# Kernel optimization log

Measured on AMD Instinct MI355X. Metric: run time of the kernel, lower is better.

## Reference

```python
import jax, jax.numpy as jnp
import numpy as np

B, S, D, H = 2, 2048, 1024, 16
DK = D // H


def setup_inputs() -> dict:
    key = jax.random.key(0)
    ks = jax.random.split(key, 12)
    sc = 1.0 / np.sqrt(D)
    return {
        "q": jax.random.normal(ks[0], (B, S, D), jnp.float32),
        "k": jax.random.normal(ks[1], (B, S, D), jnp.float32),
        "v": jax.random.normal(ks[2], (B, S, D), jnp.float32),
        "mask": jax.random.randint(ks[3], (B, S), 0, 2, jnp.int32),
        "Wq": jax.random.normal(ks[4], (D, D), jnp.float32) * sc,
        "bq": jnp.zeros((D,), jnp.float32),
        "Wk": jax.random.normal(ks[5], (D, D), jnp.float32) * sc,
        "bk": jnp.zeros((D,), jnp.float32),
        "Wv": jax.random.normal(ks[6], (D, D), jnp.float32) * sc,
        "bv": jnp.zeros((D,), jnp.float32),
        "Wo": jax.random.normal(ks[7], (D, D), jnp.float32) * sc,
        "bo": jnp.zeros((D,), jnp.float32),
    }


def reference(q, k, v, mask, Wq, bq, Wk, bk, Wv, bv, Wo, bo):
    # Projections (flax nn.Dense: x @ W + b)
    query = q @ Wq + bq          # [B,S,D]
    key_ = k @ Wk + bk
    value = v @ Wv + bv
    # split heads -> [B,H,S,DK]
    def split(x):
        return x.reshape(B, S, H, DK).transpose(0, 2, 1, 3)
    qh, kh, vh = split(query), split(key_), split(value)
    scores = jnp.einsum('bhqd,bhkd->bhqk', qh, kh) / jnp.sqrt(jnp.float32(DK))
    # Faithful to source: mask=(mask==0); where(mask==0, -1e10, scores)
    # i.e. positions where ORIGINAL mask != 0 are set to -1e10.
    m = (mask == 0)[:, None, None, :]          # [B,1,1,S] bool
    scores = jnp.where(~m, jnp.float32(-1e10), scores)
    attn = jax.nn.softmax(scores, axis=-1)     # dropout deterministic (eval)
    x = jnp.einsum('bhqk,bhkd->bhqd', attn, vh)
    x = x.transpose(0, 2, 1, 3).reshape(B, S, D)
    return x @ Wo + bo
```

## Files before the change

kernel.cpp:

```cpp
#include <hip/hip_runtime.h>
#include <hip/hip_bf16.h>

typedef unsigned short u16;
typedef unsigned int u32;
typedef __attribute__((ext_vector_type(8))) __bf16 bf16x8;
typedef __attribute__((ext_vector_type(4))) float f32x4;
typedef __attribute__((ext_vector_type(16))) float f32x16;

constexpr int Bz = 2, Sq = 2048, Dm = 1024, Hn = 16, DK = 64;

__device__ __forceinline__ u16 f2bf(float f) {
    u32 u = __builtin_bit_cast(u32, f);
    return (u16)((u + 0x7FFFu + ((u >> 16) & 1u)) >> 16);
}

__device__ __forceinline__ u32 pack_bf16(float a, float b) {
#if __has_builtin(__builtin_amdgcn_cvt_pk_bf16_f32)
    return __builtin_bit_cast(u32, __builtin_amdgcn_cvt_pk_bf16_f32(a, b));
#else
    return (u32)f2bf(a) | ((u32)f2bf(b) << 16);
#endif
}

__device__ __forceinline__ bf16x8 lds_frag(const u16* p) {
    return __builtin_bit_cast(bf16x8, *(const uint4*)p);
}
__device__ __forceinline__ bf16x8 gfrag(const u16* p) {
    return __builtin_bit_cast(bf16x8, *(const uint4*)p);
}
__device__ __forceinline__ int swz(int r) { return (r ^ (r >> 3)) & 7; }

__device__ __forceinline__ void gll16(const u16* g, u16* l) {
    __builtin_amdgcn_global_load_lds(
        (const __attribute__((address_space(1))) void*)g,
        (__attribute__((address_space(3))) void*)l, 16, 0, 0);
}

__global__ __launch_bounds__(256) void mha_prep(
    const float* __restrict__ q, const float* __restrict__ k,
    const float* __restrict__ v,
    const float* __restrict__ w0, const float* __restrict__ w1,
    const float* __restrict__ w2, const float* __restrict__ w3,
    const int* __restrict__ mask,
    u16* __restrict__ qkv_dst, u16* __restrict__ wt_dst,
    float* __restrict__ biasg, int* __restrict__ compg, int* __restrict__ nkg)
{
    __shared__ float tl[64 * 65];
    __shared__ int sc[256];
    const int z = blockIdx.z, tid = threadIdx.x;
    if (z < 3) {
        const float* s = (z == 0) ? q : (z == 1) ? k : v;
        u16* d = qkv_dst + (size_t)z * 4 * 1024 * 1024;
        size_t i = ((size_t)blockIdx.x * 256 + tid) * 8;
        float4 a = *(const float4*)(s + i);
        float4 b = *(const float4*)(s + i + 4);
        *(uint4*)(d + i) = make_uint4(pack_bf16(a.x, a.y), pack_bf16(a.z, a.w),
                                      pack_bf16(b.x, b.y), pack_bf16(b.z, b.w));
        return;
    }
    const int bx = blockIdx.x;
    if (bx >= 1026) return;
    if (bx >= 1024) {
        const int b = bx - 1024;
        const int* mp = mask + b * Sq;
        int4 m0_ = ((const int4*)mp)[tid * 2];
        int4 m1_ = ((const int4*)mp)[tid * 2 + 1];
        int a[8];
        a[0] = (m0_.x == 0); a[1] = (m0_.y == 0); a[2] = (m0_.z == 0); a[3] = (m0_.w == 0);
        a[4] = (m1_.x == 0); a[5] = (m1_.y == 0); a[6] = (m1_.z == 0); a[7] = (m1_.w == 0);
        int cnt = 0;
#pragma unroll
        for (int j = 0; j < 8; j++) cnt += a[j];
        sc[tid] = cnt;
        __syncthreads();
        for (int off = 1; off < 256; off <<= 1) {
            int u = (tid >= off) ? sc[tid - off] : 0;
            int vv = sc[tid];
            __syncthreads();
            sc[tid] = vv + u;
            __syncthreads();
        }
        const int incl = sc[tid];
        const int nk = sc[255];
        int pa = incl - cnt;
        int pi = nk + tid * 8 - pa;
        int* cp = compg + b * Sq;
        float* bbp = biasg + b * Sq;
#pragma unroll
        for (int j = 0; j < 8; j++) {
            int pos = a[j] ? pa++ : pi++;
            cp[tid * 8 + j] = pos;
            bbp[pos] = a[j] ? 0.f : -1.44269504e10f;
        }
        if (tid == 0) nkg[b] = nk;
        return;
    }
    const int zi = bx >> 8, t = bx & 255, tr = t >> 4, tc = t & 15;
    const float* src = (zi == 0) ? w0 : (zi == 1) ? w1 : (zi == 2) ? w2 : w3;
    u16* d = wt_dst + (size_t)zi * Dm * Dm;
    {
        int r = tid >> 2, cq = (tid & 3) * 16;
        const float* sp = src + (size_t)(tr * 64 + r) * Dm + tc * 64 + cq;
#pragma unroll
        for (int j = 0; j < 4; j++) {
            float4 vv = *(const float4*)(sp + j * 4);
            tl[r * 65 + cq + j * 4 + 0] = vv.x;
            tl[r * 65 + cq + j * 4 + 1] = vv.y;
            tl[r * 65 + cq + j * 4 + 2] = vv.z;
            tl[r * 65 + cq + j * 4 + 3] = vv.w;
        }
    }
    __syncthreads();
    {
        int rr = tid >> 2, cc = (tid & 3) * 16;
        u16* dp = d + (size_t)(tc * 64 + rr) * Dm + tr * 64 + cc;
        u32 px[8];
#pragma unroll
        for (int j = 0; j < 8; j++)
            px[j] = pack_bf16(tl[(cc + 2 * j) * 65 + rr], tl[(cc + 2 * j + 1) * 65 + rr]);
        *(uint4*)dp       = make_uint4(px[0], px[1], px[2], px[3]);
        *(uint4*)(dp + 8) = make_uint4(px[4], px[5], px[6], px[7]);
    }
}

__device__ __forceinline__ void gemm_core_128128(
    const u16* __restrict__ Ab, const u16* __restrict__ Bb,
    u16* As, u16* Bs, f32x4 (&acc)[4][4])
{
    const int tid = threadIdx.x, lane = tid & 63;
    const int wm = (tid >> 7) & 1, wn = (tid >> 6) & 1;
    const int frow = lane & 15, quad = lane >> 4;

#pragma unroll
    for (int mi = 0; mi < 4; mi++)
#pragma unroll
        for (int ni = 0; ni < 4; ni++) acc[mi][ni] = (f32x4){0.f, 0.f, 0.f, 0.f};

    for (int k0 = 0; k0 < 1024; k0 += 64) {
#pragma unroll
        for (int i = 0; i < 4; i++) {
            int id = tid + i * 256, r = id >> 3, c = id & 7;
            gll16(Ab + (size_t)r * 1024 + k0 + (c ^ swz(r)) * 8, As + (size_t)id * 8);
        }
#pragma unroll
        for (int i = 0; i < 4; i++) {
            int id = tid + i * 256, r = id >> 3, c = id & 7;
            gll16(Bb + (size_t)r * 1024 + k0 + (c ^ swz(r)) * 8, Bs + (size_t)id * 8);
        }
        __syncthreads();
#pragma unroll
        for (int ks = 0; ks < 2; ks++) {
            bf16x8 af[4], bfr[4];
#pragma unroll
            for (int mi = 0; mi < 4; mi++) {
                int r = wm * 64 + mi * 16 + frow;
                af[mi] = lds_frag(As + r * 64 + ((ks * 4 + quad) ^ swz(r)) * 8);
            }
#pragma unroll
            for (int ni = 0; ni < 4; ni++) {
                int r = wn * 64 + ni * 16 + frow;
                bfr[ni] = lds_frag(Bs + r * 64 + ((ks * 4 + quad) ^ swz(r)) * 8);
            }
#pragma unroll
            for (int mi = 0; mi < 4; mi++)
#pragma unroll
                for (int ni = 0; ni < 4; ni++)
                    acc[mi][ni] = __builtin_amdgcn_mfma_f32_16x16x32_bf16(
                        af[mi], bfr[ni], acc[mi][ni], 0, 0, 0);
        }
        __syncthreads();
    }
}

__device__ __forceinline__ void gemm_core_12864(
    const u16* __restrict__ Ab, const u16* __restrict__ Bb,
    u16* As, u16* Bs, f32x4 (&acc)[4][2])
{
    const int tid = threadIdx.x, lane = tid & 63;
    const int wm = (tid >> 7) & 1, wn = (tid >> 6) & 1;
    const int frow = lane & 15, quad = lane >> 4;

#pragma unroll
    for (int mi = 0; mi < 4; mi++)
#pragma unroll
        for (int ni = 0; ni < 2; ni++) acc[mi][ni] = (f32x4){0.f, 0.f, 0.f, 0.f};

    for (int k0 = 0; k0 < 1024; k0 += 64) {
#pragma unroll
        for (int i = 0; i < 4; i++) {
            int id = tid + i * 256, r = id >> 3, c = id & 7;
            gll16(Ab + (size_t)r * 1024 + k0 + (c ^ swz(r)) * 8, As + (size_t)id * 8);
        }
#pragma unroll
        for (int i = 0; i < 2; i++) {
            int id = tid + i * 256, r = id >> 3, c = id & 7;
            gll16(Bb + (size_t)r * 1024 + k0 + (c ^ swz(r)) * 8, Bs + (size_t)id * 8);
        }
        __syncthreads();
#pragma unroll
        for (int ks = 0; ks < 2; ks++) {
            bf16x8 af[4], bfr[2];
#pragma unroll
            for (int mi = 0; mi < 4; mi++) {
                int r = wm * 64 + mi * 16 + frow;
                af[mi] = lds_frag(As + r * 64 + ((ks * 4 + quad) ^ swz(r)) * 8);
            }
#pragma unroll
            for (int ni = 0; ni < 2; ni++) {
                int r = wn * 32 + ni * 16 + frow;
                bfr[ni] = lds_frag(Bs + r * 64 + ((ks * 4 + quad) ^ swz(r)) * 8);
            }
#pragma unroll
            for (int mi = 0; mi < 4; mi++)
#pragma unroll
                for (int ni = 0; ni < 2; ni++)
                    acc[mi][ni] = __builtin_amdgcn_mfma_f32_16x16x32_bf16(
                        af[mi], bfr[ni], acc[mi][ni], 0, 0, 0);
        }
        __syncthreads();
    }
}

__global__ __launch_bounds__(256, 3) void mha_proj_qkv(
    const u16* __restrict__ Qb, const u16* __restrict__ Kb, const u16* __restrict__ Vb,
    const u16* __restrict__ Wqt, const u16* __restrict__ Wkt, const u16* __restrict__ Wvt,
    const float* __restrict__ bq, const float* __restrict__ bk, const float* __restrict__ bv,
    const int* __restrict__ comp,
    u16* __restrict__ Qh, u16* __restrict__ Kh, u16* __restrict__ Vt)
{
    __shared__ __align__(16) u16 As[128 * 64];
    __shared__ __align__(16) u16 Bs[128 * 64];
    const int z = blockIdx.z, bx = blockIdx.x;
    const u16* Ab; const u16* Bb; const float* bias;
    int m0, n0;
    if (z < 2) {
        m0 = (bx & 31) * 128;
        n0 = (bx >> 5) * 128;
        Ab = ((z == 0) ? Qb : Kb) + (size_t)m0 * Dm;
        Bb = ((z == 0) ? Wqt : Wkt) + (size_t)n0 * Dm;
        bias = (z == 0) ? bq : bk;
    } else {
        m0 = (bx >> 5) * 128;
        n0 = (bx & 31) * 128;
        Ab = Wvt + (size_t)m0 * Dm;
        Bb = Vb + (size_t)n0 * Dm;
        bias = bv;
    }

    f32x4 acc[4][4];
    gemm_core_128128(Ab, Bb, As, Bs, acc);

    const int tid = threadIdx.x, lane = tid & 63;
    const int wm = (tid >> 7) & 1, wn = (tid >> 6) & 1;
    const int frow = lane & 15, quad = lane >> 4;
    u16* dstq = (z == 0) ? Qh : Kh;
#pragma unroll
    for (int mi = 0; mi < 4; mi++)
#pragma unroll
        for (int ni = 0; ni < 4; ni++)
#pragma unroll
            for (int r = 0; r < 4; r++) {
                int i = m0 + wm * 64 + mi * 16 + quad * 4 + r;
                int j = n0 + wn * 64 + ni * 16 + frow;
                if (z < 2) {
                    float val = acc[mi][ni][r] + bias[j];
                    int b = i >> 11, s = i & (Sq - 1);
                    int h = j >> 6, dk = j & (DK - 1);
                    int srow = (z == 1) ? comp[b * Sq + s] : s;
                    dstq[((size_t)(b * Hn + h) * Sq + srow) * DK + dk] = f2bf(val);
                } else {
                    float val = acc[mi][ni][r] + bias[i];
                    int h = i >> 6, dk = i & (DK - 1);
                    int bj = j >> 11, s = j & (Sq - 1);
                    int cs = comp[bj * Sq + s];
                    int sp = (cs & ~12) | ((cs & 4) << 1) | ((cs & 8) >> 1);
                    Vt[((size_t)(bj * Hn + h) * DK + dk) * Sq + sp] = f2bf(val);
                }
            }
}

__global__ __launch_bounds__(512, 4) void mha_attn(
    const u16* __restrict__ Qh, const u16* __restrict__ Kh, const u16* __restrict__ Vt,
    const float* __restrict__ biasg, const int* __restrict__ nkg,
    u16* __restrict__ X)
{
    const int bh = blockIdx.x;
    const int b = bh >> 4;
    const int q0 = blockIdx.y * 64;
    const int tid = threadIdx.x, lane = tid & 63, w = tid >> 6;
    const int wq = w & 1, p = w >> 1;
    const int qc = lane & 31, half = lane >> 5;
    constexpr float C2 = 0.125f * 1.44269504f;

    __shared__ __align__(16) u16 Ks[2][128 * 64];
    __shared__ __align__(16) u16 Vs[2][64 * 128];
    __shared__ float lsl[256];

    const u16* Qp = Qh + (size_t)bh * Sq * DK;
    const u16* Kp = Kh + (size_t)bh * Sq * DK;
    const u16* Vp = Vt + (size_t)bh * DK * Sq;
    const float* bp = biasg + b * Sq;
    const int nk = nkg[b];
    const int nt = (nk + 127) >> 7;

    bf16x8 qf[4];
    {
        const u16* qrow = Qp + (size_t)(q0 + wq * 32 + qc) * DK + half * 8;
#pragma unroll
        for (int kc = 0; kc < 4; kc++) qf[kc] = gfrag(qrow + kc * 16);
    }

    const int idA = tid, idB = tid + 512;
    const u16* ksA = Kp + (size_t)(idA >> 3) * DK + ((idA & 7) ^ swz(idA >> 3)) * 8;
    const u16* ksB = Kp + (size_t)(idB >> 3) * DK + ((idB & 7) ^ swz(idB >> 3)) * 8;
    const u16* vsA = Vp + (size_t)(idA >> 4) * Sq + (((idA & 15) ^ ((idA >> 4) & 15)) * 8);
    const u16* vsB = Vp + (size_t)(idB >> 4) * Sq + (((idB & 15) ^ ((idB >> 4) & 15)) * 8);
    u16* kdA = &Ks[0][idA * 8];
    u16* kdB = &Ks[0][idB * 8];
    u16* vdA = &Vs[0][idA * 8];
    u16* vdB = &Vs[0][idB * 8];

    auto stage = [&](int cur, int kb) {
        const int co = cur * (128 * 64);
        gll16(ksA + (size_t)kb * DK, kdA + co);
        gll16(ksB + (size_t)kb * DK, kdB + co);
        gll16(vsA + kb, vdA + co);
        gll16(vsB + kb, vdB + co);
    };

    const int kr = p * 32 + qc;
    int kfo[4];
#pragma unroll
    for (int kc = 0; kc < 4; kc++)
        kfo[kc] = kr * 64 + (((kc * 2 + half) ^ swz(kr)) * 8);
    int vfo0[2], vfo1[2];
#pragma unroll
    for (int kc = 0; kc < 2; kc++) {
        int ch = p * 4 + kc * 2 + half;
        vfo0[kc] = qc * 128 + ((ch ^ (qc & 15)) * 8);
        vfo1[kc] = (32 + qc) * 128 + ((ch ^ (qc & 15)) * 8);
    }
    const float* bpw = bp + p * 32 + 4 * half;

    float l_l = 0.f;
    f32x16 o0, o1;
#pragma unroll
    for (int i = 0; i < 16; i++) { o0[i] = 0.f; o1[i] = 0.f; }

    stage(0, 0);
    __syncthreads();

    for (int it = 0; it < nt; it++) {
        const int cur = it & 1;
        if (it + 1 < nt) stage(cur ^ 1, (it + 1) * 128);

        const u16* Kl = Ks[cur];
        const u16* Vl = Vs[cur];

        f32x16 sT;
#pragma unroll
        for (int i = 0; i < 16; i++) sT[i] = 0.f;
        __builtin_amdgcn_s_setprio(1);
#pragma unroll
        for (int kc = 0; kc < 4; kc++) {
            bf16x8 ka = lds_frag(Kl + kfo[kc]);
            sT = __builtin_amdgcn_mfma_f32_32x32x16_bf16(ka, qf[kc], sT, 0, 0, 0);
        }
        __builtin_amdgcn_s_setprio(0);

        const int kb = it * 128;
        float t[16], rs = 0.f;
#pragma unroll
        for (int g = 0; g < 4; g++) {
            float4 mb = *(const float4*)(bpw + kb + 8 * g);
#pragma unroll
            for (int r = 0; r < 4; r++) {
                float bb = (r == 0) ? mb.x : (r == 1) ? mb.y : (r == 2) ? mb.z : mb.w;
                float a = __builtin_amdgcn_exp2f(fmaf(sT[g * 4 + r], C2, bb));
                t[g * 4 + r] = a; rs += a;
            }
        }
        l_l += rs;

        u32 pk[8];
#pragma unroll
        for (int i = 0; i < 8; i++) pk[i] = pack_bf16(t[2 * i], t[2 * i + 1]);

        __builtin_amdgcn_s_setprio(1);
#pragma unroll
        for (int kc = 0; kc < 2; kc++) {
            bf16x8 pf = __builtin_bit_cast(bf16x8,
                make_uint4(pk[4 * kc], pk[4 * kc + 1], pk[4 * kc + 2], pk[4 * kc + 3]));
            bf16x8 va0 = lds_frag(Vl + vfo0[kc]);
            bf16x8 va1 = lds_frag(Vl + vfo1[kc]);
            o0 = __builtin_amdgcn_mfma_f32_32x32x16_bf16(va0, pf, o0, 0, 0, 0);
            o1 = __builtin_amdgcn_mfma_f32_32x32x16_bf16(va1, pf, o1, 0, 0, 0);
        }
        __builtin_amdgcn_s_setprio(0);
        __syncthreads();
    }

    l_l += __shfl_xor(l_l, 32);
    float* fcb = (float*)Ks;
    if (p >= 2) {
        float* fc = fcb + (size_t)(wq * 2 + (p & 1)) * 2048;
#pragma unroll
        for (int r = 0; r < 16; r++) fc[r * 64 + lane] = o0[r];
#pragma unroll
        for (int r = 0; r < 16; r++) fc[(16 + r) * 64 + lane] = o1[r];
        lsl[(wq * 2 + (p & 1)) * 64 + lane] = l_l;
    }
    __syncthreads();
    if (p < 2) {
        float* fc = fcb + (size_t)(wq * 2 + p) * 2048;
#pragma unroll
        for (int r = 0; r < 16; r++) o0[r] += fc[r * 64 + lane];
#pragma unroll
        for (int r = 0; r < 16; r++) o1[r] += fc[(16 + r) * 64 + lane];
        l_l += lsl[(wq * 2 + p) * 64 + lane];
    }
    if (p == 1) {
        float* fc = fcb + (size_t)(wq * 2 + 1) * 2048;
#pragma unroll
        for (int r = 0; r < 16; r++) fc[r * 64 + lane] = o0[r];
#pragma unroll
        for (int r = 0; r < 16; r++) fc[(16 + r) * 64 + lane] = o1[r];
        lsl[(wq * 2 + 1) * 64 + lane] = l_l;
    }
    __syncthreads();
    if (p == 0) {
        float* fc = fcb + (size_t)(wq * 2 + 1) * 2048;
#pragma unroll
        for (int r = 0; r < 16; r++) o0[r] += fc[r * 64 + lane];
#pragma unroll
        for (int r = 0; r < 16; r++) o1[r] += fc[(16 + r) * 64 + lane];
        l_l += lsl[(wq * 2 + 1) * 64 + lane];
        float inv = 1.0f / l_l;
        const int qg = q0 + wq * 32 + qc;
        u16* Xp = X + (size_t)(b * Sq + qg) * Dm + (bh & 15) * DK;
#pragma unroll
        for (int g = 0; g < 4; g++) {
            *(uint2*)&Xp[8 * g + 4 * half] =
                make_uint2(pack_bf16(o0[g * 4 + 0] * inv, o0[g * 4 + 1] * inv),
                           pack_bf16(o0[g * 4 + 2] * inv, o0[g * 4 + 3] * inv));
            *(uint2*)&Xp[32 + 8 * g + 4 * half] =
                make_uint2(pack_bf16(o1[g * 4 + 0] * inv, o1[g * 4 + 1] * inv),
                           pack_bf16(o1[g * 4 + 2] * inv, o1[g * 4 + 3] * inv));
        }
    }
}

__global__ __launch_bounds__(256) void mha_oproj(
    const u16* __restrict__ X, const u16* __restrict__ Wot,
    const float* __restrict__ bo, float* __restrict__ out)
{
    __shared__ __align__(16) u16 As[128 * 64];
    __shared__ __align__(16) u16 Bs[64 * 64];
    const int bx = blockIdx.x;
    const int m0 = (bx & 31) * 128, n0 = (bx >> 5) * 64;
    f32x4 acc[4][2];
    gemm_core_12864(X + (size_t)m0 * Dm, Wot + (size_t)n0 * Dm, As, Bs, acc);
    const int tid = threadIdx.x, lane = tid & 63;
    const int wm = (tid >> 7) & 1, wn = (tid >> 6) & 1;
    const int frow = lane & 15, quad = lane >> 4;
#pragma unroll
    for (int mi = 0; mi < 4; mi++)
#pragma unroll
        for (int ni = 0; ni < 2; ni++)
#pragma unroll
            for (int r = 0; r < 4; r++) {
                int m = m0 + wm * 64 + mi * 16 + quad * 4 + r;
                int n = n0 + wn * 32 + ni * 16 + frow;
                out[(size_t)m * Dm + n] = acc[mi][ni][r] + bo[n];
            }
}

extern "C" void kernel_launch(void* const* d_in, const int* in_sizes, int n_in,
                              void* d_out, int out_size, void* d_ws, size_t ws_size,
                              hipStream_t stream)
{
    const float* qin  = (const float*)d_in[0];
    const float* kin  = (const float*)d_in[1];
    const float* vin  = (const float*)d_in[2];
    const int*   mask = (const int*)d_in[3];
    const float* Wq   = (const float*)d_in[4];
    const float* bq   = (const float*)d_in[5];
    const float* Wk   = (const float*)d_in[6];
    const float* bk   = (const float*)d_in[7];
    const float* Wv   = (const float*)d_in[8];
    const float* bv   = (const float*)d_in[9];
    const float* Wo   = (const float*)d_in[10];
    const float* bo   = (const float*)d_in[11];
    float* out = (float*)d_out;

    u16* ws = (u16*)d_ws;
    const size_t MW = (size_t)Dm * Dm;
    const size_t MT = (size_t)Bz * Sq * Dm;
    u16* Wqt = ws;
    u16* Wkt = ws + MW;
    u16* Wvt = ws + 2 * MW;
    u16* Wot = ws + 3 * MW;
    u16* Qb  = ws + 4 * MW;
    u16* Kb  = Qb + MT;
    u16* Vb  = Kb + MT;
    u16* Qh  = Vb + MT;
    u16* Kh  = Qh + MT;
    u16* Vt  = Kh + MT;
    float* biasg = (float*)(Vt + MT);
    int*   compg = (int*)(biasg + Bz * Sq);
    int*   nkg   = (int*)(compg + Bz * Sq);
    u16* X   = Qb;

    hipLaunchKernelGGL(mha_prep, dim3(2048, 1, 4), dim3(256), 0, stream,
                       qin, kin, vin, Wq, Wk, Wv, Wo, mask, Qb, Wqt, biasg, compg, nkg);
    hipLaunchKernelGGL(mha_proj_qkv, dim3(256, 1, 3), dim3(256), 0, stream,
                       Qb, Kb, Vb, Wqt, Wkt, Wvt, bq, bk, bv, compg, Qh, Kh, Vt);
    hipLaunchKernelGGL(mha_attn, dim3(32, 32), dim3(512), 0, stream,
                       Qh, Kh, Vt, biasg, nkg, X);
    hipLaunchKernelGGL(mha_oproj, dim3(512), dim3(256), 0, stream,
                       X, Wot, bo, out);
}
```

Before: 215.2 us.

## Drop K/V double buffering in attention to raise occupancy

Replaces the double-buffered K/V shared-memory tiles with one buffer, halving LDS use. The launch-bounds occupancy hint goes from 4 to 8 blocks per CU. Each iteration now loads a tile and then synchronises before computing, so load/compute overlap inside a block is gone. The bet is that more resident blocks will hide memory latency across blocks, at the cost of stricter register limits and possible spills.

Measured after the change: 395.4 us. +83.7%, slower.

```diff
diff --git a/kernel.cpp b/kernel.cpp
--- a/kernel.cpp
+++ b/kernel.cpp
@@ -279,7 +279,7 @@
             }
 }
 
-__global__ __launch_bounds__(512, 4) void mha_attn(
+__global__ __launch_bounds__(512, 8) void mha_attn(
     const u16* __restrict__ Qh, const u16* __restrict__ Kh, const u16* __restrict__ Vt,
     const float* __restrict__ biasg, const int* __restrict__ nkg,
     u16* __restrict__ X)
@@ -292,9 +292,10 @@
     const int qc = lane & 31, half = lane >> 5;
     constexpr float C2 = 0.125f * 1.44269504f;
 
-    __shared__ __align__(16) u16 Ks[2][128 * 64];
-    __shared__ __align__(16) u16 Vs[2][64 * 128];
+    __shared__ __align__(16) u16 SB[128 * 64 + 64 * 128];
     __shared__ float lsl[256];
+    u16* Ks = SB;
+    u16* Vs = SB + 128 * 64;
 
     const u16* Qp = Qh + (size_t)bh * Sq * DK;
     const u16* Kp = Kh + (size_t)bh * Sq * DK;
@@ -315,17 +316,16 @@
     const u16* ksB = Kp + (size_t)(idB >> 3) * DK + ((idB & 7) ^ swz(idB >> 3)) * 8;
     const u16* vsA = Vp + (size_t)(idA >> 4) * Sq + (((idA & 15) ^ ((idA >> 4) & 15)) * 8);
     const u16* vsB = Vp + (size_t)(idB >> 4) * Sq + (((idB & 15) ^ ((idB >> 4) & 15)) * 8);
-    u16* kdA = &Ks[0][idA * 8];
-    u16* kdB = &Ks[0][idB * 8];
-    u16* vdA = &Vs[0][idA * 8];
-    u16* vdB = &Vs[0][idB * 8];
-
-    auto stage = [&](int cur, int kb) {
-        const int co = cur * (128 * 64);
-        gll16(ksA + (size_t)kb * DK, kdA + co);
-        gll16(ksB + (size_t)kb * DK, kdB + co);
-        gll16(vsA + kb, vdA + co);
-        gll16(vsB + kb, vdB + co);
+    u16* kdA = Ks + idA * 8;
+    u16* kdB = Ks + idB * 8;
+    u16* vdA = Vs + idA * 8;
+    u16* vdB = Vs + idB * 8;
+
+    auto stage = [&](int kb) {
+        gll16(ksA + (size_t)kb * DK, kdA);
+        gll16(ksB + (size_t)kb * DK, kdB);
+        gll16(vsA + kb, vdA);
+        gll16(vsB + kb, vdB);
     };
 
     const int kr = p * 32 + qc;
@@ -347,15 +347,9 @@
 #pragma unroll
     for (int i = 0; i < 16; i++) { o0[i] = 0.f; o1[i] = 0.f; }
 
-    stage(0, 0);
-    __syncthreads();
-
     for (int it = 0; it < nt; it++) {
-        const int cur = it & 1;
-        if (it + 1 < nt) stage(cur ^ 1, (it + 1) * 128);
-
-        const u16* Kl = Ks[cur];
-        const u16* Vl = Vs[cur];
+        stage(it * 128);
+        __syncthreads();
 
         f32x16 sT;
 #pragma unroll
@@ -363,7 +357,7 @@
         __builtin_amdgcn_s_setprio(1);
 #pragma unroll
         for (int kc = 0; kc < 4; kc++) {
-            bf16x8 ka = lds_frag(Kl + kfo[kc]);
+            bf16x8 ka = lds_frag(Ks + kfo[kc]);
             sT = __builtin_amdgcn_mfma_f32_32x32x16_bf16(ka, qf[kc], sT, 0, 0, 0);
         }
         __builtin_amdgcn_s_setprio(0);
@@ -391,8 +385,8 @@
         for (int kc = 0; kc < 2; kc++) {
             bf16x8 pf = __builtin_bit_cast(bf16x8,
                 make_uint4(pk[4 * kc], pk[4 * kc + 1], pk[4 * kc + 2], pk[4 * kc + 3]));
-            bf16x8 va0 = lds_frag(Vl + vfo0[kc]);
-            bf16x8 va1 = lds_frag(Vl + vfo1[kc]);
+            bf16x8 va0 = lds_frag(Vs + vfo0[kc]);
+            bf16x8 va1 = lds_frag(Vs + vfo1[kc]);
             o0 = __builtin_amdgcn_mfma_f32_32x32x16_bf16(va0, pf, o0, 0, 0, 0);
             o1 = __builtin_amdgcn_mfma_f32_32x32x16_bf16(va1, pf, o1, 0, 0, 0);
         }
@@ -401,7 +395,7 @@
     }
 
     l_l += __shfl_xor(l_l, 32);
-    float* fcb = (float*)Ks;
+    float* fcb = (float*)SB;
     if (p >= 2) {
         float* fc = fcb + (size_t)(wq * 2 + (p & 1)) * 2048;
 #pragma unroll
```
